# Performance work log

Measured on AMD Instinct MI355X. Metric: run time of the kernel, lower is better.

Reference implementation:

```python
import jax, jax.numpy as jnp
import numpy as np

NUM_ROUTE_NODES = 1152
IN_CHANNELS = 8
OUT_CHANNELS = 16
NUM_DIGITS = 10
NUM_ITERATIONS = 3
BATCH = 256


def squash(x):
    # Faithful to the original: uses the GLOBAL norm of the whole tensor,
    # not a per-capsule norm.
    norm = jnp.linalg.norm(x)
    sq = norm * norm
    return (sq / (1.0 + sq)) * (x / norm)


def setup_inputs() -> dict:
    key = jax.random.key(0)
    k_u, k_w = jax.random.split(key)
    u = jax.random.normal(k_u, (BATCH, NUM_ROUTE_NODES, IN_CHANNELS), dtype=jnp.float32)
    # W: (1, R, D, out, in) as in nn.Parameter(torch.randn(...))
    W = jax.random.normal(k_w, (1, NUM_ROUTE_NODES, NUM_DIGITS, OUT_CHANNELS, IN_CHANNELS), dtype=jnp.float32)
    return {"u": u, "W": W}


def reference(u, W):
    # u_hat[b,r,d,o] = sum_i W[0,r,d,o,i] * u[b,r,i]
    u_hat = jnp.einsum('rdoi,bri->brdo', W[0], u)  # (B, R, D, O)
    R, D = u_hat.shape[1], u_hat.shape[2]
    b = jnp.zeros((R, D), dtype=u_hat.dtype)
    v = None
    for _ in range(NUM_ITERATIONS):
        c = jax.nn.softmax(b, axis=1)[None, :, :, None]     # (1, R, D, 1)
        s = jnp.sum(u_hat * c, axis=1)                      # (B, D, O)
        v = squash(s)                                       # (B, D, O)
        # agreement: a[b,r,d] = sum_o u_hat[b,r,d,o] * v[b,d,o]
        a = jnp.einsum('brdo,bdo->brd', u_hat, v)           # (B, R, D)
        b = b + jnp.sum(a, axis=0)                          # (R, D)
    return v
```

## Files before the change

### kernel.cpp

```cpp
#include <hip/hip_runtime.h>
#include <math.h>

#define R_NODES 1152
#define DIGITS 10
#define OUT_CH 16
#define IN_CH 8
#define BATCH 256
#define COLS 160
#define W_PER_R 1280
#define NSPLIT 72
#define RPS 16
#define YB_S 8
#define YBLK 8
#define UP 88
#define AB_STRIDE (YBLK * R_NODES * DIGITS)

typedef __attribute__((ext_vector_type(8))) short short8v;
typedef __attribute__((ext_vector_type(4))) float floatx4;

__device__ inline unsigned short f2bf(float x) {
    union { float f; unsigned int i; } v; v.f = x;
    unsigned int r = v.i + 0x7FFFu + ((v.i >> 16) & 1u);
    return (unsigned short)(r >> 16);
}
__device__ inline float bf2f(unsigned short x) {
    union { unsigned int i; float f; } v; v.i = ((unsigned int)x) << 16;
    return v.f;
}

__global__ __launch_bounds__(256, 3) void k_s(
    const float* __restrict__ u,
    const float* __restrict__ W,
    const float* __restrict__ ab,
    unsigned short* __restrict__ part,
    float* __restrict__ sq,
    int nbuf)
{
    __shared__ unsigned short ulds[32 * UP];
    __shared__ unsigned short wlds[COLS * UP];
    __shared__ float cs[RPS * DIGITS];

    const int split = blockIdx.x;
    const int b0 = blockIdx.y * 32;
    const int t = threadIdx.x;
    const int r0 = split * RPS;

    if (split == 0 && blockIdx.y == 0 && t == 0) *sq = 0.f;

    if (t < RPS * DIGITS) {
        float a = 0.f;
        int r_l = t / 10, d = t - r_l * 10;
        const float* p0 = ab + (size_t)(r0 + r_l) * DIGITS + d;
        for (int bu = 0; bu < nbuf; ++bu)
#pragma unroll
            for (int yy = 0; yy < YBLK; ++yy)
                a += p0[(size_t)bu * AB_STRIDE + (size_t)yy * (R_NODES * DIGITS)];
        cs[t] = a;
    }
    __syncthreads();
    if (t < RPS) {
        float e[DIGITS];
        float m = -1e30f;
#pragma unroll
        for (int d = 0; d < DIGITS; ++d) m = fmaxf(m, cs[t*10 + d]);
        float ssum = 0.f;
#pragma unroll
        for (int d = 0; d < DIGITS; ++d) { e[d] = expf(cs[t*10 + d] - m); ssum += e[d]; }
        float inv = 1.f / ssum;
#pragma unroll
        for (int d = 0; d < DIGITS; ++d) cs[t*10 + d] = e[d] * inv;
    }
    __syncthreads();

    const int w = t >> 6, l = t & 63;
    const int mtile = w & 1;
    const int ncol0 = (w >> 1) * 5;
    const int koff = (l >> 4) * 8;
    const int arow = (mtile * 16 + (l & 15)) * UP;

    floatx4 acc[5];
#pragma unroll
    for (int j = 0; j < 5; ++j) acc[j] = (floatx4){0.f, 0.f, 0.f, 0.f};

    for (int ch = 0; ch < 2; ++ch) {
        const int rc = r0 + ch * 8;
        float4 uv[2];
#pragma unroll
        for (int p = 0; p < 2; ++p) {
            int idx = t + p * 256;
            int b = idx >> 4, q = idx & 15;
            uv[p] = *(const float4*)(u + (size_t)(b0 + b) * (R_NODES * IN_CH)
                                       + (size_t)rc * IN_CH + q * 4);
        }
        float4 wr[10];
        {
            const float4* Wg = (const float4*)(W + (size_t)rc * W_PER_R);
#pragma unroll
            for (int p = 0; p < 10; ++p) wr[p] = Wg[t + p * 256];
        }
        if (ch) __syncthreads();
#pragma unroll
        for (int p = 0; p < 2; ++p) {
            int idx = t + p * 256;
            int b = idx >> 4, q = idx & 15;
            *(short4*)&ulds[b * UP + q * 4] =
                make_short4((short)f2bf(uv[p].x), (short)f2bf(uv[p].y),
                            (short)f2bf(uv[p].z), (short)f2bf(uv[p].w));
        }
#pragma unroll
        for (int p = 0; p < 10; ++p) {
            int e4 = t + p * 256;
            int e  = e4 * 4;
            int r_l = e4 / 320;
            int rem = e - r_l * W_PER_R;
            int col = rem >> 3;
            int i0  = e & 7;
            float cv = cs[(ch * 8 + r_l) * 10 + (rem >> 7)];
            float4 w4 = wr[p];
            *(short4*)&wlds[col * UP + r_l * 8 + i0] =
                make_short4((short)f2bf(w4.x * cv), (short)f2bf(w4.y * cv),
                            (short)f2bf(w4.z * cv), (short)f2bf(w4.w * cv));
        }
        __syncthreads();
        short8v a0 = *(const short8v*)&ulds[arow + koff];
        short8v a1 = *(const short8v*)&ulds[arow + 32 + koff];
#pragma unroll
        for (int j = 0; j < 5; ++j) {
            const int bcol = ((ncol0 + j) * 16 + (l & 15)) * UP;
            short8v bb0 = *(const short8v*)&wlds[bcol + koff];
            short8v bb1 = *(const short8v*)&wlds[bcol + 32 + koff];
            acc[j] = __builtin_amdgcn_mfma_f32_16x16x32_bf16(a0, bb0, acc[j], 0, 0, 0);
            acc[j] = __builtin_amdgcn_mfma_f32_16x16x32_bf16(a1, bb1, acc[j], 0, 0, 0);
        }
    }

    unsigned short* pp = part + (size_t)split * (BATCH * COLS);
    const int gb = b0 + mtile * 16 + (l >> 4) * 4;
#pragma unroll
    for (int j = 0; j < 5; ++j) {
        const int gc = (ncol0 + j) * 16 + (l & 15);
#pragma unroll
        for (int reg = 0; reg < 4; ++reg)
            pp[(size_t)(gb + reg) * COLS + gc] = f2bf(acc[j][reg]);
    }
}

__global__ void k_sq(const unsigned short* __restrict__ part,
                     float* __restrict__ s,
                     float* __restrict__ sq)
{
    const int t = threadIdx.x;
    const int e0 = blockIdx.x * 64;
    const int el = t & 63, q = t >> 6;
    float v = 0.f;
    for (int sp = q; sp < NSPLIT; sp += 4)
        v += bf2f(part[(size_t)sp * (BATCH * COLS) + e0 + el]);
    __shared__ float red[256];
    red[t] = v;
    __syncthreads();
    if (t < 64) {
        float vv = red[t] + red[t + 64] + red[t + 128] + red[t + 192];
        s[e0 + t] = vv;
        float x = vv * vv;
#pragma unroll
        for (int off = 32; off > 0; off >>= 1)
            x += __shfl_down(x, off, 64);
        if (t == 0) atomicAdd(sq, x);
    }
}

__global__ __launch_bounds__(256) void k_a(
    const float* __restrict__ u,
    const float* __restrict__ W,
    const float* __restrict__ s,
    const float* __restrict__ sq,
    float* __restrict__ ab)
{
    __shared__ float st[32 * COLS];
    __shared__ float ut[32 * 64];
    const int t = threadIdx.x;
    const int rblk = blockIdx.x;
    const int r = rblk * 8 + (t >> 5);
    const int tt = t & 31;
    const int bstart = blockIdx.y * 32;

    {
        const float4* sp = (const float4*)(s + (size_t)bstart * COLS);
#pragma unroll
        for (int p = 0; p < 5; ++p) ((float4*)st)[t + p * 256] = sp[t + p * 256];
    }
#pragma unroll
    for (int p = 0; p < 2; ++p) {
        int idx = t + p * 256;
        int bb = idx >> 4, qq = idx & 15;
        ((float4*)ut)[idx] =
            ((const float4*)(u + (size_t)(bstart + bb) * (R_NODES*IN_CH) + (size_t)rblk * 64))[qq];
    }

    float wreg[5][8];
#pragma unroll
    for (int k = 0; k < 5; ++k) {
        const float4* wp = (const float4*)(W + (size_t)r * W_PER_R + (size_t)(tt + 32*k) * IN_CH);
        float4 w0 = wp[0], w1 = wp[1];
        wreg[k][0]=w0.x; wreg[k][1]=w0.y; wreg[k][2]=w0.z; wreg[k][3]=w0.w;
        wreg[k][4]=w1.x; wreg[k][5]=w1.y; wreg[k][6]=w1.z; wreg[k][7]=w1.w;
    }
    __syncthreads();

    float acc[5] = {0.f, 0.f, 0.f, 0.f, 0.f};
#pragma unroll 2
    for (int b = 0; b < 32; ++b) {
        const float* ub = &ut[b * 64 + (t >> 5) * 8];
        float4 a0 = *(const float4*)ub;
        float4 a1 = *(const float4*)(ub + 4);
        const float* sb = &st[b * COLS];
#pragma unroll
        for (int k = 0; k < 5; ++k) {
            float vv = sb[tt + 32*k];
            float uh;
            uh = wreg[k][0] * a0.x;
            uh = fmaf(wreg[k][1], a0.y, uh);
            uh = fmaf(wreg[k][2], a0.z, uh);
            uh = fmaf(wreg[k][3], a0.w, uh);
            uh = fmaf(wreg[k][4], a1.x, uh);
            uh = fmaf(wreg[k][5], a1.y, uh);
            uh = fmaf(wreg[k][6], a1.z, uh);
            uh = fmaf(wreg[k][7], a1.w, uh);
            acc[k] = fmaf(uh, vv, acc[k]);
        }
    }
    float q = *sq;
    float scale = sqrtf(q) / (1.f + q);
    float* abp = ab + (size_t)blockIdx.y * (R_NODES * DIGITS) + r * DIGITS;
#pragma unroll
    for (int k = 0; k < 5; ++k) {
        float x = acc[k] * scale;
        x += __shfl_xor(x, 1, 64);
        x += __shfl_xor(x, 2, 64);
        x += __shfl_xor(x, 4, 64);
        x += __shfl_xor(x, 8, 64);
        if ((tt & 15) == 0) {
            int d = (tt >> 4) + 2*k;
            abp[d] = x;
        }
    }
}

__global__ void k_scale(const float* __restrict__ s,
                        const float* __restrict__ sq,
                        float* __restrict__ out)
{
    int e = blockIdx.x * 256 + threadIdx.x;
    float q = *sq;
    float scale = sqrtf(q) / (1.f + q);
    out[e] = s[e] * scale;
}

extern "C" void kernel_launch(void* const* d_in, const int* in_sizes, int n_in,
                              void* d_out, int out_size, void* d_ws, size_t ws_size,
                              hipStream_t stream)
{
    const float* u = (const float*)d_in[0];
    const float* W = (const float*)d_in[1];
    float* out = (float*)d_out;
    float* ws = (float*)d_ws;

    float* s    = ws;
    float* sq   = ws + 40960;
    float* ab   = ws + 41024;
    unsigned short* part = (unsigned short*)(ws + 41024 + 2 * AB_STRIDE);

    for (int it = 0; it < 3; ++it) {
        k_s<<<dim3(NSPLIT, YB_S), dim3(256), 0, stream>>>(u, W, ab, part, sq, it);
        k_sq<<<dim3(BATCH * COLS / 64), dim3(256), 0, stream>>>(part, s, sq);
        if (it < 2)
            k_a<<<dim3(R_NODES / 8, YBLK), dim3(256), 0, stream>>>(u, W, s, sq,
                                                                   ab + (size_t)it * AB_STRIDE);
        else
            k_scale<<<dim3(BATCH * COLS / 256), dim3(256), 0, stream>>>(s, sq, out);
    }
}
```

Before: 102.5 us.

## Reassociate agreement as s^T·u product via bf16 MFMA, contract with W in routing kernel

The agreement step no longer recomputes u_hat per batch. It first forms M[d,o,r,i] = sum_b s[b,d,o]·u[b,r,i] with bf16 MFMA instructions in a new kernel. The logit update is then obtained inside k_s by contracting M with W and the per-iteration squash scale, and per-iteration squared norms are kept in a small buffer. This swaps the FP32 FMA-heavy k_a for a tensor-core GEMM plus a larger M intermediate (1.47M floats per iteration). It also adds bf16 rounding error to the routing logits and extra global reads of M and W in k_s.

```diff
diff --git a/kernel.cpp b/kernel.cpp
--- a/kernel.cpp
+++ b/kernel.cpp
@@ -8,12 +8,13 @@
 #define BATCH 256
 #define COLS 160
 #define W_PER_R 1280
+#define MROW 9216
+#define MSTRIDE (COLS * MROW)
 #define NSPLIT 72
 #define RPS 16
 #define YB_S 8
-#define YBLK 8
 #define UP 88
-#define AB_STRIDE (YBLK * R_NODES * DIGITS)
+#define KST 264
 
 typedef __attribute__((ext_vector_type(8))) short short8v;
 typedef __attribute__((ext_vector_type(4))) float floatx4;
@@ -31,9 +32,10 @@
 __global__ __launch_bounds__(256, 3) void k_s(
     const float* __restrict__ u,
     const float* __restrict__ W,
-    const float* __restrict__ ab,
+    const float* __restrict__ Mb,
+    const float* __restrict__ sqbuf,
     unsigned short* __restrict__ part,
-    float* __restrict__ sq,
+    float* __restrict__ sqz,
     int nbuf)
 {
     __shared__ unsigned short ulds[32 * UP];
@@ -45,16 +47,28 @@
     const int t = threadIdx.x;
     const int r0 = split * RPS;
 
-    if (split == 0 && blockIdx.y == 0 && t == 0) *sq = 0.f;
+    if (split == 0 && blockIdx.y == 0 && t == 0) *sqz = 0.f;
 
     if (t < RPS * DIGITS) {
         float a = 0.f;
         int r_l = t / 10, d = t - r_l * 10;
-        const float* p0 = ab + (size_t)(r0 + r_l) * DIGITS + d;
-        for (int bu = 0; bu < nbuf; ++bu)
-#pragma unroll
-            for (int yy = 0; yy < YBLK; ++yy)
-                a += p0[(size_t)bu * AB_STRIDE + (size_t)yy * (R_NODES * DIGITS)];
+        const float* Wrow = W + (size_t)(r0 + r_l) * W_PER_R + d * 128;
+        for (int bu = 0; bu < nbuf; ++bu) {
+            float q = sqbuf[bu];
+            float sc = sqrtf(q) / (1.f + q);
+            const float* Mrow = Mb + (size_t)bu * MSTRIDE
+                                   + (size_t)(d * 16) * MROW + (size_t)(r0 + r_l) * 8;
+            float partial = 0.f;
+#pragma unroll
+            for (int o = 0; o < 16; ++o) {
+                const float4* wv = (const float4*)(Wrow + o * 8);
+                const float4* mv = (const float4*)(Mrow + (size_t)o * MROW);
+                float4 w0 = wv[0], w1 = wv[1], m0 = mv[0], m1 = mv[1];
+                partial += w0.x*m0.x + w0.y*m0.y + w0.z*m0.z + w0.w*m0.w
+                         + w1.x*m1.x + w1.y*m1.y + w1.z*m1.z + w1.w*m1.w;
+            }
+            a += sc * partial;
+        }
         cs[t] = a;
     }
     __syncthreads();
@@ -169,81 +183,53 @@
     }
 }
 
-__global__ __launch_bounds__(256) void k_a(
+__global__ __launch_bounds__(256, 3) void k_m(
     const float* __restrict__ u,
-    const float* __restrict__ W,
     const float* __restrict__ s,
-    const float* __restrict__ sq,
-    float* __restrict__ ab)
-{
-    __shared__ float st[32 * COLS];
-    __shared__ float ut[32 * 64];
+    float* __restrict__ M)
+{
+    __shared__ unsigned short sld[16 * KST];
+    __shared__ unsigned short uld[64 * KST];
     const int t = threadIdx.x;
-    const int rblk = blockIdx.x;
-    const int r = rblk * 8 + (t >> 5);
-    const int tt = t & 31;
-    const int bstart = blockIdx.y * 32;
-
-    {
-        const float4* sp = (const float4*)(s + (size_t)bstart * COLS);
-#pragma unroll
-        for (int p = 0; p < 5; ++p) ((float4*)st)[t + p * 256] = sp[t + p * 256];
-    }
-#pragma unroll
-    for (int p = 0; p < 2; ++p) {
+    const int rig = blockIdx.x;
+    const int do0 = blockIdx.y * 16;
+
+#pragma unroll
+    for (int p = 0; p < 4; ++p) {
         int idx = t + p * 256;
-        int bb = idx >> 4, qq = idx & 15;
-        ((float4*)ut)[idx] =
-            ((const float4*)(u + (size_t)(bstart + bb) * (R_NODES*IN_CH) + (size_t)rblk * 64))[qq];
-    }
-
-    float wreg[5][8];
-#pragma unroll
-    for (int k = 0; k < 5; ++k) {
-        const float4* wp = (const float4*)(W + (size_t)r * W_PER_R + (size_t)(tt + 32*k) * IN_CH);
-        float4 w0 = wp[0], w1 = wp[1];
-        wreg[k][0]=w0.x; wreg[k][1]=w0.y; wreg[k][2]=w0.z; wreg[k][3]=w0.w;
-        wreg[k][4]=w1.x; wreg[k][5]=w1.y; wreg[k][6]=w1.z; wreg[k][7]=w1.w;
-    }
-    __syncthreads();
-
-    float acc[5] = {0.f, 0.f, 0.f, 0.f, 0.f};
-#pragma unroll 2
-    for (int b = 0; b < 32; ++b) {
-        const float* ub = &ut[b * 64 + (t >> 5) * 8];
-        float4 a0 = *(const float4*)ub;
-        float4 a1 = *(const float4*)(ub + 4);
-        const float* sb = &st[b * COLS];
-#pragma unroll
-        for (int k = 0; k < 5; ++k) {
-            float vv = sb[tt + 32*k];
-            float uh;
-            uh = wreg[k][0] * a0.x;
-            uh = fmaf(wreg[k][1], a0.y, uh);
-            uh = fmaf(wreg[k][2], a0.z, uh);
-            uh = fmaf(wreg[k][3], a0.w, uh);
-            uh = fmaf(wreg[k][4], a1.x, uh);
-            uh = fmaf(wreg[k][5], a1.y, uh);
-            uh = fmaf(wreg[k][6], a1.z, uh);
-            uh = fmaf(wreg[k][7], a1.w, uh);
-            acc[k] = fmaf(uh, vv, acc[k]);
-        }
-    }
-    float q = *sq;
-    float scale = sqrtf(q) / (1.f + q);
-    float* abp = ab + (size_t)blockIdx.y * (R_NODES * DIGITS) + r * DIGITS;
-#pragma unroll
-    for (int k = 0; k < 5; ++k) {
-        float x = acc[k] * scale;
-        x += __shfl_xor(x, 1, 64);
-        x += __shfl_xor(x, 2, 64);
-        x += __shfl_xor(x, 4, 64);
-        x += __shfl_xor(x, 8, 64);
-        if ((tt & 15) == 0) {
-            int d = (tt >> 4) + 2*k;
-            abp[d] = x;
-        }
-    }
+        int b = idx >> 2, q = idx & 3;
+        float4 v = *(const float4*)(s + (size_t)b * COLS + do0 + q * 4);
+        sld[(q*4+0)*KST + b] = f2bf(v.x);
+        sld[(q*4+1)*KST + b] = f2bf(v.y);
+        sld[(q*4+2)*KST + b] = f2bf(v.z);
+        sld[(q*4+3)*KST + b] = f2bf(v.w);
+    }
+#pragma unroll
+    for (int p = 0; p < 16; ++p) {
+        int idx = t + p * 256;
+        int b = idx >> 4, q = idx & 15;
+        float4 v = *(const float4*)(u + (size_t)b * MROW + rig * 64 + q * 4);
+        uld[(q*4+0)*KST + b] = f2bf(v.x);
+        uld[(q*4+1)*KST + b] = f2bf(v.y);
+        uld[(q*4+2)*KST + b] = f2bf(v.z);
+        uld[(q*4+3)*KST + b] = f2bf(v.w);
+    }
+    __syncthreads();
+
+    const int w = t >> 6, l = t & 63;
+    floatx4 acc = {0.f, 0.f, 0.f, 0.f};
+#pragma unroll
+    for (int ks = 0; ks < 8; ++ks) {
+        int koff = ks * 32 + (l >> 4) * 8;
+        short8v av = *(const short8v*)&sld[(l & 15) * KST + koff];
+        short8v bv = *(const short8v*)&uld[(w * 16 + (l & 15)) * KST + koff];
+        acc = __builtin_amdgcn_mfma_f32_16x16x32_bf16(av, bv, acc, 0, 0, 0);
+    }
+    const int ri = rig * 64 + w * 16 + (l & 15);
+    const int dor = do0 + (l >> 4) * 4;
+#pragma unroll
+    for (int reg = 0; reg < 4; ++reg)
+        M[(size_t)(dor + reg) * MROW + ri] = acc[reg];
 }
 
 __global__ void k_scale(const float* __restrict__ s,
@@ -265,18 +251,18 @@
     float* out = (float*)d_out;
     float* ws = (float*)d_ws;
 
-    float* s    = ws;
-    float* sq   = ws + 40960;
-    float* ab   = ws + 41024;
-    unsigned short* part = (unsigned short*)(ws + 41024 + 2 * AB_STRIDE);
+    float* s     = ws;
+    float* sqbuf = ws + 40960;
+    float* M     = ws + 41024;
+    unsigned short* part = (unsigned short*)(ws + 41024 + 2 * MSTRIDE);
 
     for (int it = 0; it < 3; ++it) {
-        k_s<<<dim3(NSPLIT, YB_S), dim3(256), 0, stream>>>(u, W, ab, part, sq, it);
-        k_sq<<<dim3(BATCH * COLS / 64), dim3(256), 0, stream>>>(part, s, sq);
+        k_s<<<dim3(NSPLIT, YB_S), dim3(256), 0, stream>>>(u, W, M, sqbuf, part,
+                                                          sqbuf + it, it);
+        k_sq<<<dim3(BATCH * COLS / 64), dim3(256), 0, stream>>>(part, s, sqbuf + it);
         if (it < 2)
-            k_a<<<dim3(R_NODES / 8, YBLK), dim3(256), 0, stream>>>(u, W, s, sq,
-                                                                   ab + (size_t)it * AB_STRIDE);
+            k_m<<<dim3(144, 10), dim3(256), 0, stream>>>(u, s, M + (size_t)it * MSTRIDE);
         else
-            k_scale<<<dim3(BATCH * COLS / 256), dim3(256), 0, stream>>>(s, sq, out);
-    }
-}
+            k_scale<<<dim3(BATCH * COLS / 256), dim3(256), 0, stream>>>(s, sqbuf + 2, out);
+    }
+}
```

New measurement: 135.2 us. 1.32x slower.
